# Kernel optimization log

Measured on AMD Instinct MI355X. Metric: run time of the kernel, lower is better.

The kernel has to match this reference:

```python
import jax, jax.numpy as jnp
import numpy as np

EPS = 1e-5


def grid_sample_bilinear_border(img, grid):
    """PyTorch F.grid_sample(mode='bilinear', padding_mode='border', align_corners=False).
    img: [B,C,H,W], grid: [B,Hg,Wg,2] with (x,y) in [-1,1]. Returns [B,C,Hg,Wg]."""
    B, C, H, W = img.shape
    gx, gy = grid[..., 0], grid[..., 1]
    # unnormalize (align_corners=False), then border-clamp the coordinate
    ix = jnp.clip((gx + 1.0) * (W * 0.5) - 0.5, 0.0, W - 1.0)
    iy = jnp.clip((gy + 1.0) * (H * 0.5) - 0.5, 0.0, H - 1.0)
    x0f = jnp.floor(ix)
    y0f = jnp.floor(iy)
    wx = ix - x0f  # [B,Hg,Wg]
    wy = iy - y0f
    x0 = jnp.clip(x0f.astype(jnp.int32), 0, W - 1)
    y0 = jnp.clip(y0f.astype(jnp.int32), 0, H - 1)
    x1 = jnp.clip(x0 + 1, 0, W - 1)
    y1 = jnp.clip(y0 + 1, 0, H - 1)

    def gather(im, y, x):  # im [C,H,W]; y,x [Hg,Wg] -> [C,Hg,Wg]
        return im[:, y, x]

    g = jax.vmap(gather)
    v00 = g(img, y0, x0)
    v01 = g(img, y0, x1)
    v10 = g(img, y1, x0)
    v11 = g(img, y1, x1)
    wx = wx[:, None]  # [B,1,Hg,Wg]
    wy = wy[:, None]
    return (v00 * (1 - wx) * (1 - wy) + v01 * wx * (1 - wy)
            + v10 * (1 - wx) * wy + v11 * wx * wy)


def bn_relu(x, gamma, beta, mean, var):
    # x: [B,Cc,N,H,W]; per-channel inference batchnorm + relu
    shape = (1, -1, 1, 1, 1)
    inv = gamma * jax.lax.rsqrt(var + EPS)
    return jax.nn.relu(x * inv.reshape(shape) + (beta - mean * inv).reshape(shape))


def setup_inputs() -> dict:
    key = jax.random.key(0)
    ks = jax.random.split(key, 16)
    B, C, H, W = 4, 64, 256, 320
    N, G = 9, 8
    return {
        "ref_feature": jax.random.normal(ks[0], (B, C, H, W), jnp.float32),
        "grid": jax.random.uniform(ks[1], (B, N * H, W, 2), jnp.float32, minval=-1.0, maxval=1.0),
        "conv0_w": jax.random.normal(ks[2], (16, G), jnp.float32) * 0.2,
        "bn0_gamma": jax.random.uniform(ks[3], (16,), jnp.float32, minval=0.5, maxval=1.5),
        "bn0_beta": jax.random.normal(ks[4], (16,), jnp.float32) * 0.1,
        "bn0_mean": jax.random.normal(ks[5], (16,), jnp.float32) * 0.1,
        "bn0_var": jax.random.uniform(ks[6], (16,), jnp.float32, minval=0.5, maxval=1.5),
        "conv1_w": jax.random.normal(ks[7], (8, 16), jnp.float32) * 0.2,
        "bn1_gamma": jax.random.uniform(ks[8], (8,), jnp.float32, minval=0.5, maxval=1.5),
        "bn1_beta": jax.random.normal(ks[9], (8,), jnp.float32) * 0.1,
        "bn1_mean": jax.random.normal(ks[10], (8,), jnp.float32) * 0.1,
        "bn1_var": jax.random.uniform(ks[11], (8,), jnp.float32, minval=0.5, maxval=1.5),
        "sim_w": jax.random.normal(ks[12], (1, 8), jnp.float32) * 0.2,
        "sim_b": jax.random.normal(ks[13], (1,), jnp.float32) * 0.1,
    }


def reference(ref_feature, grid, conv0_w, bn0_gamma, bn0_beta, bn0_mean, bn0_var,
              conv1_w, bn1_gamma, bn1_beta, bn1_mean, bn1_var, sim_w, sim_b):
    B, C, H, W = ref_feature.shape
    G = 8
    N = grid.shape[1] // H  # neighbors
    Cg = C // G
    # irregular bilinear gather: [B,C,N*H,W] -> [B,G,Cg,N,H,W]
    sampled = grid_sample_bilinear_border(ref_feature, grid).reshape(B, G, Cg, N, H, W)
    ref = ref_feature.reshape(B, G, Cg, H, W)[:, :, :, None]  # [B,G,Cg,1,H,W]
    weight = (sampled * ref).mean(axis=2)  # group similarity, [B,G,N,H,W]
    # 1x1x1 conv stack (conv-bn-relu x2, then conv + sigmoid)
    x = bn_relu(jnp.einsum('og,bgnhw->bonhw', conv0_w, weight),
                bn0_gamma, bn0_beta, bn0_mean, bn0_var)
    x = bn_relu(jnp.einsum('oc,bcnhw->bonhw', conv1_w, x),
                bn1_gamma, bn1_beta, bn1_mean, bn1_var)
    sim = jnp.einsum('oc,bcnhw->bonhw', sim_w, x) + sim_b.reshape(1, -1, 1, 1, 1)
    return jax.nn.sigmoid(sim[:, 0])  # [B,N,H,W]
```

## Files before the change

### kernel.cpp

```cpp
#include <hip/hip_runtime.h>
#include <hip/hip_fp16.h>

#define B_ 4
#define C_ 64
#define H_ 256
#define W_ 320
#define N_ 9
#define TOT (B_*N_*H_*W_)
#define HW_ (H_*W_)
#define HWC (H_*W_*C_)

#define NHWC_HALFS (B_*H_*W_*C_)
#define PRM_OFF_BYTES (NHWC_HALFS*2)

union H2x4U { float4 f; __half2 h[4]; };

__global__ __launch_bounds__(512) void fold_params(
    const float* __restrict__ w0, const float* __restrict__ g0, const float* __restrict__ be0,
    const float* __restrict__ mu0, const float* __restrict__ va0,
    const float* __restrict__ w1, const float* __restrict__ g1, const float* __restrict__ be1,
    const float* __restrict__ mu1, const float* __restrict__ va1,
    const float* __restrict__ sw, const float* __restrict__ sb, float* __restrict__ prm)
{
    int t = threadIdx.x;
    if (t < 128) {
        int o = t >> 3;
        float a = g0[o] / sqrtf(va0[o] + 1e-5f);
        prm[t] = w0[t] * a;
    } else if (t < 144) {
        int o = t - 128;
        float a = g0[o] / sqrtf(va0[o] + 1e-5f);
        prm[128 + o] = be0[o] - mu0[o] * a;
    } else if (t < 272) {
        int i = t - 144;
        int c = i >> 4;
        float a = g1[c] / sqrtf(va1[c] + 1e-5f);
        prm[144 + i] = w1[i] * a;
    } else if (t < 280) {
        int c = t - 272;
        float a = g1[c] / sqrtf(va1[c] + 1e-5f);
        prm[272 + c] = be1[c] - mu1[c] * a;
    } else if (t < 288) {
        prm[t] = sw[t - 280];
    } else if (t == 288) {
        prm[288] = sb[0];
    }
}

__global__ __launch_bounds__(256) void nchw_to_nhwc_fp16(const float* __restrict__ in,
                                                         __half* __restrict__ out)
{
    __shared__ unsigned int tile[64 * 34];
    const int blk = blockIdx.x;
    const int b   = blk / (HW_ / 64);
    const int hw0 = (blk % (HW_ / 64)) * 64;
    const int tid = threadIdx.x;
    const int px  = tid & 63;
    const int q   = tid >> 6;

    const float* src = in + (size_t)b * HWC + hw0;
#pragma unroll
    for (int i = 0; i < 8; ++i) {
        int c = i * 8 + q * 2;
        float f0 = src[(size_t)c * HW_ + px];
        float f1 = src[(size_t)(c + 1) * HW_ + px];
        __half2 h = __floats2half2_rn(f0, f1);
        tile[px * 34 + (c >> 1)] = *(unsigned int*)&h;
    }
    __syncthreads();

    __half* dstbase = out + ((size_t)b * HW_ + hw0) * C_;
#pragma unroll
    for (int j = 0; j < 2; ++j) {
        int p  = j * 32 + (tid >> 3);
        int cg = tid & 7;
        const unsigned int* r = &tile[p * 34 + cg * 4];
        uint4 v;
        v.x = r[0]; v.y = r[1]; v.z = r[2]; v.w = r[3];
        *(uint4*)(dstbase + (size_t)p * C_ + cg * 8) = v;
    }
}

__device__ __forceinline__ __half2 bl_acc(__half2 a00, __half2 a01, __half2 a10, __half2 a11,
                                          __half2 r, __half2 wxh, __half2 wyh, __half2 acc)
{
    __half2 top = __hfma2(wxh, __hsub2(a01, a00), a00);
    __half2 bot = __hfma2(wxh, __hsub2(a11, a10), a10);
    __half2 s   = __hfma2(wyh, __hsub2(bot, top), top);
    return __hfma2(s, r, acc);
}

__device__ __forceinline__ float gd_compute(const H2x4U& r, const H2x4U& v00, const H2x4U& v01,
                                            const H2x4U& v10, const H2x4U& v11, float wx, float wy)
{
    __half2 wxh = __float2half2_rn(wx);
    __half2 wyh = __float2half2_rn(wy);
    __half2 acc = __float2half2_rn(0.f);
    acc = bl_acc(v00.h[0], v01.h[0], v10.h[0], v11.h[0], r.h[0], wxh, wyh, acc);
    acc = bl_acc(v00.h[1], v01.h[1], v10.h[1], v11.h[1], r.h[1], wxh, wyh, acc);
    acc = bl_acc(v00.h[2], v01.h[2], v10.h[2], v11.h[2], r.h[2], wxh, wyh, acc);
    acc = bl_acc(v00.h[3], v01.h[3], v10.h[3], v11.h[3], r.h[3], wxh, wyh, acc);
    float2 f = __half22float2(acc);
    return (f.x + f.y) * 0.125f;
}

__global__ __launch_bounds__(256) void fwn_main(const __half* __restrict__ img,
                                                const float* __restrict__ grid,
                                                const float* __restrict__ prm,
                                                float* __restrict__ out)
{
    __shared__ float wlds[256][9];
    __shared__ int   ash[256 * 9];
    const int tid  = threadIdx.x;
    const int lane = tid & 63;
    const int wv   = tid >> 6;
    const int g    = lane & 7;
    const int sub  = lane >> 3;
    const int pix0 = blockIdx.x * 256;
    const int g8   = g * 8;

    {
        int P = pix0 + tid;
        float2 gxy = ((const float2*)grid)[P];
        float ix = fminf(fmaxf((gxy.x + 1.f) * (W_ * 0.5f) - 0.5f, 0.f), (float)(W_ - 1));
        float iy = fminf(fmaxf((gxy.y + 1.f) * (H_ * 0.5f) - 0.5f, 0.f), (float)(H_ - 1));
        float x0f = floorf(ix), y0f = floorf(iy);
        int x0 = (int)x0f, y0 = (int)y0f;
        int dx = (x0 < W_ - 1) ? C_ : 0;
        int dy = (y0 < H_ - 1) ? W_ * C_ : 0;

        unsigned up = (unsigned)P;
        unsigned w_ = up % W_;
        unsigned t1 = up / W_;
        unsigned h_ = t1 & (H_ - 1);
        unsigned b_ = (t1 >> 8) / N_;

        int base = (int)(b_ * HWC);
        int r9 = tid * 9;
        ash[r9 + 0] = base + (y0 * W_ + x0) * C_;
        ash[r9 + 1] = dx;
        ash[r9 + 2] = dy;
        ash[r9 + 3] = base + (int)(h_ * W_ + w_) * C_;
        ash[r9 + 4] = __float_as_int(ix - x0f);
        ash[r9 + 5] = __float_as_int(iy - y0f);
    }
    __syncthreads();

#pragma unroll
    for (int pp = 0; pp < 8; pp += 2) {
        const int rA = (wv * 64 + pp * 8 + sub) * 9;
        const int rB = rA + 8 * 9;

        int oA  = ash[rA + 0] + g8;
        int dxA = ash[rA + 1];
        int dyA = ash[rA + 2];
        int orA = ash[rA + 3] + g8;
        float wxA = __int_as_float(ash[rA + 4]);
        float wyA = __int_as_float(ash[rA + 5]);
        H2x4U ra, a00, a01, a10, a11;
        ra.f  = *(const float4*)(img + orA);
        a00.f = *(const float4*)(img + oA);
        a01.f = *(const float4*)(img + oA + dxA);
        a10.f = *(const float4*)(img + oA + dyA);
        a11.f = *(const float4*)(img + oA + dxA + dyA);

        int oB  = ash[rB + 0] + g8;
        int dxB = ash[rB + 1];
        int dyB = ash[rB + 2];
        int orB = ash[rB + 3] + g8;
        float wxB = __int_as_float(ash[rB + 4]);
        float wyB = __int_as_float(ash[rB + 5]);
        H2x4U rb, b00, b01, b10, b11;
        rb.f  = *(const float4*)(img + orB);
        b00.f = *(const float4*)(img + oB);
        b01.f = *(const float4*)(img + oB + dxB);
        b10.f = *(const float4*)(img + oB + dyB);
        b11.f = *(const float4*)(img + oB + dxB + dyB);

        wlds[wv * 64 + pp * 8 + sub][g]     = gd_compute(ra, a00, a01, a10, a11, wxA, wyA);
        wlds[wv * 64 + pp * 8 + sub + 8][g] = gd_compute(rb, b00, b01, b10, b11, wxB, wyB);
    }

    __syncthreads();

    float wv8[8];
#pragma unroll
    for (int i = 0; i < 8; ++i) wv8[i] = wlds[tid][i];

    float h0[16];
#pragma unroll
    for (int o = 0; o < 16; ++o) {
        float a = prm[128 + o];
#pragma unroll
        for (int gg = 0; gg < 8; ++gg) a = fmaf(prm[o * 8 + gg], wv8[gg], a);
        h0[o] = fmaxf(a, 0.f);
    }
    float s = prm[288];
#pragma unroll
    for (int c = 0; c < 8; ++c) {
        float a = prm[272 + c];
#pragma unroll
        for (int o = 0; o < 16; ++o) a = fmaf(prm[144 + c * 16 + o], h0[o], a);
        float h1 = fmaxf(a, 0.f);
        s = fmaf(prm[280 + c], h1, s);
    }
    out[pix0 + tid] = 1.f / (1.f + __expf(-s));
}

extern "C" void kernel_launch(void* const* d_in, const int* in_sizes, int n_in,
                              void* d_out, int out_size, void* d_ws, size_t ws_size,
                              hipStream_t stream)
{
    const float* ref   = (const float*)d_in[0];
    const float* grd   = (const float*)d_in[1];
    const float* w0    = (const float*)d_in[2];
    const float* g0    = (const float*)d_in[3];
    const float* be0   = (const float*)d_in[4];
    const float* mu0   = (const float*)d_in[5];
    const float* va0   = (const float*)d_in[6];
    const float* w1    = (const float*)d_in[7];
    const float* g1    = (const float*)d_in[8];
    const float* be1   = (const float*)d_in[9];
    const float* mu1   = (const float*)d_in[10];
    const float* va1   = (const float*)d_in[11];
    const float* sw    = (const float*)d_in[12];
    const float* sb    = (const float*)d_in[13];
    float* out = (float*)d_out;

    __half* img = (__half*)d_ws;
    float* prm  = (float*)((char*)d_ws + PRM_OFF_BYTES);

    fold_params<<<1, 512, 0, stream>>>(w0, g0, be0, mu0, va0, w1, g1, be1, mu1, va1, sw, sb, prm);
    nchw_to_nhwc_fp16<<<B_ * (HW_ / 64), 256, 0, stream>>>(ref, img);
    fwn_main<<<TOT / 256, 256, 0, stream>>>(img, grd, prm, out);
}
```

Baseline: 321.2 us.

## Loop over neighbors per block to reuse reference features in registers

After: 364.4 us. 13.5% more time.

```diff
diff --git a/kernel.cpp b/kernel.cpp
--- a/kernel.cpp
+++ b/kernel.cpp
@@ -104,10 +104,10 @@
     return (f.x + f.y) * 0.125f;
 }
 
-__global__ __launch_bounds__(256) void fwn_main(const __half* __restrict__ img,
-                                                const float* __restrict__ grid,
-                                                const float* __restrict__ prm,
-                                                float* __restrict__ out)
+__global__ __launch_bounds__(256, 5) void fwn_main(const __half* __restrict__ img,
+                                                   const float* __restrict__ grid,
+                                                   const float* __restrict__ prm,
+                                                   float* __restrict__ out)
 {
     __shared__ float wlds[256][9];
     __shared__ int   ash[256 * 9];
@@ -116,95 +116,80 @@
     const int wv   = tid >> 6;
     const int g    = lane & 7;
     const int sub  = lane >> 3;
-    const int pix0 = blockIdx.x * 256;
     const int g8   = g * 8;
-
-    {
-        int P = pix0 + tid;
-        float2 gxy = ((const float2*)grid)[P];
-        float ix = fminf(fmaxf((gxy.x + 1.f) * (W_ * 0.5f) - 0.5f, 0.f), (float)(W_ - 1));
-        float iy = fminf(fmaxf((gxy.y + 1.f) * (H_ * 0.5f) - 0.5f, 0.f), (float)(H_ - 1));
-        float x0f = floorf(ix), y0f = floorf(iy);
-        int x0 = (int)x0f, y0 = (int)y0f;
-        int dx = (x0 < W_ - 1) ? C_ : 0;
-        int dy = (y0 < H_ - 1) ? W_ * C_ : 0;
-
-        unsigned up = (unsigned)P;
-        unsigned w_ = up % W_;
-        unsigned t1 = up / W_;
-        unsigned h_ = t1 & (H_ - 1);
-        unsigned b_ = (t1 >> 8) / N_;
-
-        int base = (int)(b_ * HWC);
-        int r9 = tid * 9;
-        ash[r9 + 0] = base + (y0 * W_ + x0) * C_;
-        ash[r9 + 1] = dx;
-        ash[r9 + 2] = dy;
-        ash[r9 + 3] = base + (int)(h_ * W_ + w_) * C_;
-        ash[r9 + 4] = __float_as_int(ix - x0f);
-        ash[r9 + 5] = __float_as_int(iy - y0f);
-    }
-    __syncthreads();
-
-#pragma unroll
-    for (int pp = 0; pp < 8; pp += 2) {
-        const int rA = (wv * 64 + pp * 8 + sub) * 9;
-        const int rB = rA + 8 * 9;
-
-        int oA  = ash[rA + 0] + g8;
-        int dxA = ash[rA + 1];
-        int dyA = ash[rA + 2];
-        int orA = ash[rA + 3] + g8;
-        float wxA = __int_as_float(ash[rA + 4]);
-        float wyA = __int_as_float(ash[rA + 5]);
-        H2x4U ra, a00, a01, a10, a11;
-        ra.f  = *(const float4*)(img + orA);
-        a00.f = *(const float4*)(img + oA);
-        a01.f = *(const float4*)(img + oA + dxA);
-        a10.f = *(const float4*)(img + oA + dyA);
-        a11.f = *(const float4*)(img + oA + dxA + dyA);
-
-        int oB  = ash[rB + 0] + g8;
-        int dxB = ash[rB + 1];
-        int dyB = ash[rB + 2];
-        int orB = ash[rB + 3] + g8;
-        float wxB = __int_as_float(ash[rB + 4]);
-        float wyB = __int_as_float(ash[rB + 5]);
-        H2x4U rb, b00, b01, b10, b11;
-        rb.f  = *(const float4*)(img + orB);
-        b00.f = *(const float4*)(img + oB);
-        b01.f = *(const float4*)(img + oB + dxB);
-        b10.f = *(const float4*)(img + oB + dyB);
-        b11.f = *(const float4*)(img + oB + dxB + dyB);
-
-        wlds[wv * 64 + pp * 8 + sub][g]     = gd_compute(ra, a00, a01, a10, a11, wxA, wyA);
-        wlds[wv * 64 + pp * 8 + sub + 8][g] = gd_compute(rb, b00, b01, b10, b11, wxB, wyB);
-    }
-
-    __syncthreads();
-
-    float wv8[8];
-#pragma unroll
-    for (int i = 0; i < 8; ++i) wv8[i] = wlds[tid][i];
-
-    float h0[16];
-#pragma unroll
-    for (int o = 0; o < 16; ++o) {
-        float a = prm[128 + o];
-#pragma unroll
-        for (int gg = 0; gg < 8; ++gg) a = fmaf(prm[o * 8 + gg], wv8[gg], a);
-        h0[o] = fmaxf(a, 0.f);
-    }
-    float s = prm[288];
-#pragma unroll
-    for (int c = 0; c < 8; ++c) {
-        float a = prm[272 + c];
-#pragma unroll
-        for (int o = 0; o < 16; ++o) a = fmaf(prm[144 + c * 16 + o], h0[o], a);
-        float h1 = fmaxf(a, 0.f);
-        s = fmaf(prm[280 + c], h1, s);
-    }
-    out[pix0 + tid] = 1.f / (1.f + __expf(-s));
+    const int b    = blockIdx.x / (HW_ / 256);
+    const int hwb  = (blockIdx.x % (HW_ / 256)) * 256;
+    const int ibase = b * HWC;
+
+    H2x4U refr[8];
+#pragma unroll
+    for (int pp = 0; pp < 8; ++pp) {
+        int px = wv * 64 + pp * 8 + sub;
+        refr[pp].f = *(const float4*)(img + ibase + (hwb + px) * C_ + g8);
+    }
+
+    const float2* gbase = (const float2*)grid + (size_t)b * (N_ * HW_) + hwb;
+    float* obase = out + (size_t)b * (N_ * HW_) + hwb;
+
+    for (int n = 0; n < N_; ++n) {
+        {
+            float2 gxy = gbase[n * HW_ + tid];
+            float ix = fminf(fmaxf((gxy.x + 1.f) * (W_ * 0.5f) - 0.5f, 0.f), (float)(W_ - 1));
+            float iy = fminf(fmaxf((gxy.y + 1.f) * (H_ * 0.5f) - 0.5f, 0.f), (float)(H_ - 1));
+            float x0f = floorf(ix), y0f = floorf(iy);
+            int x0 = (int)x0f, y0 = (int)y0f;
+            int dx = (x0 < W_ - 1) ? C_ : 0;
+            int dy = (y0 < H_ - 1) ? W_ * C_ : 0;
+            int r9 = tid * 9;
+            ash[r9 + 0] = ibase + (y0 * W_ + x0) * C_;
+            ash[r9 + 1] = dx;
+            ash[r9 + 2] = dy;
+            ash[r9 + 3] = __float_as_int(ix - x0f);
+            ash[r9 + 4] = __float_as_int(iy - y0f);
+        }
+        __syncthreads();
+
+#pragma unroll
+        for (int pp = 0; pp < 8; ++pp) {
+            int px = wv * 64 + pp * 8 + sub;
+            int r9 = px * 9;
+            int o  = ash[r9 + 0] + g8;
+            int dx = ash[r9 + 1];
+            int dy = ash[r9 + 2];
+            float wx = __int_as_float(ash[r9 + 3]);
+            float wy = __int_as_float(ash[r9 + 4]);
+            H2x4U v00, v01, v10, v11;
+            v00.f = *(const float4*)(img + o);
+            v01.f = *(const float4*)(img + o + dx);
+            v10.f = *(const float4*)(img + o + dy);
+            v11.f = *(const float4*)(img + o + dx + dy);
+            wlds[px][g] = gd_compute(refr[pp], v00, v01, v10, v11, wx, wy);
+        }
+        __syncthreads();
+
+        float wv8[8];
+#pragma unroll
+        for (int i = 0; i < 8; ++i) wv8[i] = wlds[tid][i];
+
+        float h0[16];
+#pragma unroll
+        for (int o = 0; o < 16; ++o) {
+            float a = prm[128 + o];
+#pragma unroll
+            for (int gg = 0; gg < 8; ++gg) a = fmaf(prm[o * 8 + gg], wv8[gg], a);
+            h0[o] = fmaxf(a, 0.f);
+        }
+        float s = prm[288];
+#pragma unroll
+        for (int c = 0; c < 8; ++c) {
+            float a = prm[272 + c];
+#pragma unroll
+            for (int o = 0; o < 16; ++o) a = fmaf(prm[144 + c * 16 + o], h0[o], a);
+            float h1 = fmaxf(a, 0.f);
+            s = fmaf(prm[280 + c], h1, s);
+        }
+        obase[n * HW_ + tid] = 1.f / (1.f + __expf(-s));
+    }
 }
 
 extern "C" void kernel_launch(void* const* d_in, const int* in_sizes, int n_in,
@@ -232,5 +217,5 @@
 
     fold_params<<<1, 512, 0, stream>>>(w0, g0, be0, mu0, va0, w1, g1, be1, mu1, va1, sw, sb, prm);
     nchw_to_nhwc_fp16<<<B_ * (HW_ / 64), 256, 0, stream>>>(ref, img);
-    fwn_main<<<TOT / 256, 256, 0, stream>>>(img, grd, prm, out);
-}
+    fwn_main<<<B_ * (HW_ / 256), 256, 0, stream>>>(img, grd, prm, out);
+}
```
